# Kernel tuning notes

Hardware: AMD Instinct MI355X
Metric: run time of the kernel (lower is better)

## Reference

```python
import jax, jax.numpy as jnp
import numpy as np

B, S, D, H = 2, 2048, 1024, 16
DK = D // H  # 64


def setup_inputs() -> dict:
    key = jax.random.key(0)
    ks = jax.random.split(key, 12)
    def lin(kw, kb, fan_in, shape_w):
        bound = 1.0 / np.sqrt(fan_in)
        W = jax.random.uniform(kw, shape_w, jnp.float32, -bound, bound)
        b = jax.random.uniform(kb, (shape_w[0],), jnp.float32, -bound, bound)
        return W, b
    Q = jax.random.normal(ks[0], (B, S, D), jnp.float32)
    K = jax.random.normal(ks[1], (B, S, D), jnp.float32)
    V = jax.random.normal(ks[2], (B, S, D), jnp.float32)
    attn_mask = jax.random.randint(ks[3], (B, S, S), 0, 2) == 1  # bool, True=masked
    Wq, bq = lin(ks[4], ks[5], D, (D, D))
    Wk, bk = lin(ks[6], ks[7], D, (D, D))
    Wv, bv = lin(ks[8], ks[9], D, (D, D))
    Wo, bo = lin(ks[10], ks[11], D, (D, D))
    return {"Q": Q, "K": K, "V": V, "attn_mask": attn_mask,
            "Wq": Wq, "bq": bq, "Wk": Wk, "bk": bk,
            "Wv": Wv, "bv": bv, "Wo": Wo, "bo": bo}


def reference(Q, K, V, attn_mask, Wq, bq, Wk, bk, Wv, bv, Wo, bo):
    b, s, d = Q.shape
    # project and split heads: [B,S,D] -> [B,H,S,DK]
    def heads(x, W, bias):
        y = x @ W.T + bias
        return y.reshape(b, -1, H, DK).transpose(0, 2, 1, 3)
    q = heads(Q, Wq, bq)
    k = heads(K, Wk, bk)
    v = heads(V, Wv, bv)
    # scaled dot-product attention with custom reweighting
    scores = jnp.einsum('bhqd,bhkd->bhqk', q, k) / np.sqrt(DK).astype(jnp.float32)
    scores = jnp.where(attn_mask[:, None, :, :], jnp.float32(-1e9), scores)
    attn_weights = jax.nn.softmax(scores, axis=-1) * scores.shape[-1]  # non-standard *S_k scale
    ctx = jnp.einsum('bhqk,bhkd->bhqd', attn_weights, v)
    ctx = ctx.transpose(0, 2, 1, 3).reshape(b, -1, H * DK)
    output = ctx @ Wo.T + bo
    return output, attn_weights
```

## Files before the change

kernel.cpp:

```cpp
#include <hip/hip_runtime.h>
#include <hip/hip_bf16.h>
#include <type_traits>

typedef __bf16 bf16_t;
typedef __attribute__((ext_vector_type(8))) __bf16 bf16x8;
typedef __attribute__((ext_vector_type(4))) float f32x4;

#define B_ 2
#define S_ 2048
#define D_ 1024
#define H_ 16
#define DK_ 64

enum { OM_F32 = 0, OM_BF16 = 1, OM_SPLIT = 2, OM_HEADT = 3 };

__device__ inline void split8(const float* __restrict__ p, bf16x8& h, bf16x8& l) {
    float4 x0 = *(const float4*)p;
    float4 x1 = *(const float4*)(p + 4);
    float xs[8] = {x0.x, x0.y, x0.z, x0.w, x1.x, x1.y, x1.z, x1.w};
#pragma unroll
    for (int i = 0; i < 8; ++i) {
        bf16_t hh = (bf16_t)xs[i];
        h[i] = hh;
        l[i] = (bf16_t)(xs[i] - (float)hh);
    }
}
__device__ inline void hi8(const float* __restrict__ p, bf16x8& h) {
    float4 x0 = *(const float4*)p;
    float4 x1 = *(const float4*)(p + 4);
    float xs[8] = {x0.x, x0.y, x0.z, x0.w, x1.x, x1.y, x1.z, x1.w};
#pragma unroll
    for (int i = 0; i < 8; ++i) h[i] = (bf16_t)xs[i];
}

template <typename AT, int OMODE, bool SPLIT>
__global__ __launch_bounds__(256) void gemm_bt(
    const AT* __restrict__ A,
    const float* __restrict__ W,
    const float* __restrict__ bias,
    void* __restrict__ Yp,
    void* __restrict__ Y2p,
    int M, int N, int K)
{
    const int NB = N >> 6;
    const int bm = blockIdx.x / NB;
    const int bn = blockIdx.x % NB;
    const int tid  = threadIdx.x;
    const int wave = tid >> 6;
    const int lane = tid & 63;
    const int l16  = lane & 15;
    const int quad = lane >> 4;
    const int wm = wave >> 1, wn = wave & 1;

    __shared__ bf16_t Ah[64][40];
    __shared__ bf16_t Wh[64][40];
    __shared__ bf16_t Al[SPLIT ? 64 : 1][40];
    __shared__ bf16_t Wl[SPLIT ? 64 : 1][40];

    const int srow = tid >> 2;
    const int scol = (tid & 3) * 8;

    f32x4 acc[2][2];
#pragma unroll
    for (int i = 0; i < 2; ++i)
#pragma unroll
        for (int j = 0; j < 2; ++j) acc[i][j] = (f32x4){0.f, 0.f, 0.f, 0.f};

    const AT*    Arow = A + (size_t)(bm * 64 + srow) * K + scol;
    const float* Wrow = W + (size_t)(bn * 64 + srow) * K + scol;

    for (int k0 = 0; k0 < K; k0 += 32) {
        if constexpr (std::is_same_v<AT, float>) {
            bf16x8 ah, al;
            if constexpr (SPLIT) {
                split8(Arow + k0, ah, al);
                *(bf16x8*)(&Al[srow][scol]) = al;
            } else {
                hi8(Arow + k0, ah);
            }
            *(bf16x8*)(&Ah[srow][scol]) = ah;
        } else {
            *(bf16x8*)(&Ah[srow][scol]) = *(const bf16x8*)(Arow + k0);
        }
        {
            bf16x8 wh, wl;
            if constexpr (SPLIT) {
                split8(Wrow + k0, wh, wl);
                *(bf16x8*)(&Wl[srow][scol]) = wl;
            } else {
                hi8(Wrow + k0, wh);
            }
            *(bf16x8*)(&Wh[srow][scol]) = wh;
        }
        __syncthreads();

        bf16x8 afh[2], bfh[2], afl[2], bfl[2];
#pragma unroll
        for (int mi = 0; mi < 2; ++mi) {
            afh[mi] = *(const bf16x8*)(&Ah[wm * 32 + mi * 16 + l16][quad * 8]);
            if constexpr (SPLIT)
                afl[mi] = *(const bf16x8*)(&Al[wm * 32 + mi * 16 + l16][quad * 8]);
        }
#pragma unroll
        for (int ni = 0; ni < 2; ++ni) {
            bfh[ni] = *(const bf16x8*)(&Wh[wn * 32 + ni * 16 + l16][quad * 8]);
            if constexpr (SPLIT)
                bfl[ni] = *(const bf16x8*)(&Wl[wn * 32 + ni * 16 + l16][quad * 8]);
        }

#pragma unroll
        for (int mi = 0; mi < 2; ++mi)
#pragma unroll
            for (int ni = 0; ni < 2; ++ni) {
                acc[mi][ni] = __builtin_amdgcn_mfma_f32_16x16x32_bf16(
                    afh[mi], bfh[ni], acc[mi][ni], 0, 0, 0);
                if constexpr (SPLIT) {
                    acc[mi][ni] = __builtin_amdgcn_mfma_f32_16x16x32_bf16(
                        afl[mi], bfh[ni], acc[mi][ni], 0, 0, 0);
                    acc[mi][ni] = __builtin_amdgcn_mfma_f32_16x16x32_bf16(
                        afh[mi], bfl[ni], acc[mi][ni], 0, 0, 0);
                }
            }
        __syncthreads();
    }

#pragma unroll
    for (int ni = 0; ni < 2; ++ni) {
        const int col = bn * 64 + wn * 32 + ni * 16 + l16;
        const float bv = bias[col];
#pragma unroll
        for (int mi = 0; mi < 2; ++mi) {
#pragma unroll
            for (int r = 0; r < 4; ++r) {
                const int row = bm * 64 + wm * 32 + mi * 16 + quad * 4 + r;
                const float v = acc[mi][ni][r] + bv;
                if constexpr (OMODE == OM_F32) {
                    ((float*)Yp)[(size_t)row * N + col] = v;
                } else if constexpr (OMODE == OM_BF16) {
                    ((bf16_t*)Yp)[(size_t)row * N + col] = (bf16_t)v;
                } else if constexpr (OMODE == OM_SPLIT) {
                    const bf16_t hh = (bf16_t)v;
                    ((bf16_t*)Yp)[(size_t)row * N + col] = hh;
                    ((bf16_t*)Y2p)[(size_t)row * N + col] = (bf16_t)(v - (float)hh);
                } else {
                    const int bb  = row >> 11;
                    const int ss  = row & (S_ - 1);
                    const int hh2 = col >> 6;
                    const int dk  = col & (DK_ - 1);
                    ((bf16_t*)Yp)[((size_t)((bb * H_ + hh2) * DK_ + dk) << 11) + ss] =
                        (bf16_t)v;
                }
            }
        }
    }
}

__global__ __launch_bounds__(256) void pack_mask(
    const int* __restrict__ mask,
    unsigned long long* __restrict__ pk)
{
    const size_t nwords = (size_t)B_ * S_ * S_ / 64;
    const int lane = threadIdx.x & 63;
    size_t w = (size_t)blockIdx.x * 4 + (threadIdx.x >> 6);
    const size_t stride = (size_t)gridDim.x * 4;
    for (; w < nwords; w += stride) {
        const int m = mask[w * 64 + lane];
        const unsigned long long bb = __ballot(m != 0);
        if (lane == 0) pk[w] = bb;
    }
}

__global__ __launch_bounds__(256) void attn_kernel(
    const bf16_t* __restrict__ qh_g,
    const bf16_t* __restrict__ ql_g,
    const bf16_t* __restrict__ kh_g,
    const bf16_t* __restrict__ kl_g,
    const bf16_t* __restrict__ vt_g,
    const unsigned* __restrict__ pm,
    float* __restrict__ wout,
    float* __restrict__ normbuf,
    bf16_t* __restrict__ ctx)
{
    const int bid = blockIdx.x;
    const int qt = bid & 31;
    const int h  = (bid >> 5) & 15;
    const int b  = bid >> 9;
    const int tid  = threadIdx.x;
    const int wave = tid >> 6;
    const int lane = tid & 63;
    const int l16  = lane & 15;
    const int quad = lane >> 4;

    const int q0 = qt * 64 + wave * 16;

    __shared__ bf16_t Kh[32][72];
    __shared__ bf16_t Kl[32][72];
    __shared__ bf16_t vT[64][40];
    __shared__ bf16_t wl[4][16][40];

    const size_t qoff = ((size_t)(b * S_ + q0 + l16)) * D_ + h * DK_ + quad * 8;
    const bf16x8 qh0 = *(const bf16x8*)(qh_g + qoff);
    const bf16x8 qh1 = *(const bf16x8*)(qh_g + qoff + 32);
    const bf16x8 ql0 = *(const bf16x8*)(ql_g + qoff);
    const bf16x8 ql1 = *(const bf16x8*)(ql_g + qoff + 32);

    const float scale = 0.125f;

    const int srow  = tid >> 3;
    const int scol  = (tid & 7) * 8;
    const int srow2 = tid >> 2;
    const int scol2 = (tid & 3) * 8;
    const bf16_t* khst = kh_g + (size_t)b * S_ * D_ + h * DK_;
    const bf16_t* klst = kl_g + (size_t)b * S_ * D_ + h * DK_;
    const bf16_t* vtst = vt_g + ((size_t)(b * H_ + h) * DK_ + srow2) * S_ + scol2;

    const unsigned* pmrow = pm + (size_t)b * S_ * (S_ / 32);
    const size_t wbase = ((size_t)(b * H_ + h)) * S_ * S_;

    float lsum[4] = {0.f, 0.f, 0.f, 0.f};
    f32x4 acc[4];
#pragma unroll
    for (int t = 0; t < 4; ++t) acc[t] = (f32x4){0.f, 0.f, 0.f, 0.f};

    for (int j0 = 0; j0 < S_; j0 += 32) {
        {
            const size_t ko = (size_t)(j0 + srow) * D_ + scol;
            *(bf16x8*)(&Kh[srow][scol]) = *(const bf16x8*)(khst + ko);
            *(bf16x8*)(&Kl[srow][scol]) = *(const bf16x8*)(klst + ko);
            *(bf16x8*)(&vT[srow2][scol2]) = *(const bf16x8*)(vtst + j0);
        }
        unsigned mw[4];
#pragma unroll
        for (int r = 0; r < 4; ++r) {
            const int q = q0 + quad * 4 + r;
            mw[r] = pmrow[(size_t)q * (S_ / 32) + (j0 >> 5)];
        }
        __syncthreads();

#pragma unroll
        for (int sub = 0; sub < 2; ++sub) {
            const int rr = sub * 16 + l16;
            const bf16x8 kh0 = *(const bf16x8*)(&Kh[rr][quad * 8]);
            const bf16x8 kh1 = *(const bf16x8*)(&Kh[rr][32 + quad * 8]);
            const bf16x8 kl0 = *(const bf16x8*)(&Kl[rr][quad * 8]);
            const bf16x8 kl1 = *(const bf16x8*)(&Kl[rr][32 + quad * 8]);
            f32x4 c = (f32x4){0.f, 0.f, 0.f, 0.f};
            c = __builtin_amdgcn_mfma_f32_16x16x32_bf16(qh0, kh0, c, 0, 0, 0);
            c = __builtin_amdgcn_mfma_f32_16x16x32_bf16(qh1, kh1, c, 0, 0, 0);
            c = __builtin_amdgcn_mfma_f32_16x16x32_bf16(ql0, kh0, c, 0, 0, 0);
            c = __builtin_amdgcn_mfma_f32_16x16x32_bf16(ql1, kh1, c, 0, 0, 0);
            c = __builtin_amdgcn_mfma_f32_16x16x32_bf16(qh0, kl0, c, 0, 0, 0);
            c = __builtin_amdgcn_mfma_f32_16x16x32_bf16(qh1, kl1, c, 0, 0, 0);
            const int jt = j0 + sub * 16;
#pragma unroll
            for (int r = 0; r < 4; ++r) {
                const int q = q0 + quad * 4 + r;
                const int msk = (mw[r] >> (sub * 16 + l16)) & 1;
                const float e = msk ? 0.f : __expf(c[r] * scale);
                lsum[r] += e;
                __builtin_nontemporal_store(e, &wout[wbase + (size_t)q * S_ + jt + l16]);
                wl[wave][quad * 4 + r][sub * 16 + l16] = (bf16_t)e;
            }
        }
        const bf16x8 wa = *(const bf16x8*)(&wl[wave][l16][quad * 8]);
#pragma unroll
        for (int t = 0; t < 4; ++t) {
            const bf16x8 vf = *(const bf16x8*)(&vT[t * 16 + l16][quad * 8]);
            acc[t] = __builtin_amdgcn_mfma_f32_16x16x32_bf16(wa, vf, acc[t], 0, 0, 0);
        }
        __syncthreads();
    }

#pragma unroll
    for (int r = 0; r < 4; ++r) {
        float v = lsum[r];
        v += __shfl_xor(v, 1);
        v += __shfl_xor(v, 2);
        v += __shfl_xor(v, 4);
        v += __shfl_xor(v, 8);
        lsum[r] = v;
    }
    float norm[4];
#pragma unroll
    for (int r = 0; r < 4; ++r) norm[r] = 2048.f / lsum[r];

    if (l16 == 0) {
#pragma unroll
        for (int r = 0; r < 4; ++r)
            normbuf[(size_t)(b * H_ + h) * S_ + q0 + quad * 4 + r] = norm[r];
    }

#pragma unroll
    for (int t = 0; t < 4; ++t) {
#pragma unroll
        for (int r = 0; r < 4; ++r) {
            const int q = q0 + quad * 4 + r;
            ctx[((size_t)(b * S_ + q)) * D_ + h * DK_ + t * 16 + l16] =
                (bf16_t)(acc[t][r] * norm[r]);
        }
    }
}

__global__ __launch_bounds__(256) void rescale_wout(
    float* __restrict__ wout,
    const float* __restrict__ normbuf)
{
    const size_t total = (size_t)B_ * H_ * S_ * (S_ / 4);
    f32x4* wp = (f32x4*)wout;
    for (size_t i = (size_t)blockIdx.x * blockDim.x + threadIdx.x;
         i < total;
         i += (size_t)gridDim.x * blockDim.x) {
        const float n = normbuf[i >> 9];
        f32x4 w = __builtin_nontemporal_load(wp + i);
        w *= n;
        __builtin_nontemporal_store(w, wp + i);
    }
}

extern "C" void kernel_launch(void* const* d_in, const int* in_sizes, int n_in,
                              void* d_out, int out_size, void* d_ws, size_t ws_size,
                              hipStream_t stream) {
    const float* Q    = (const float*)d_in[0];
    const float* K    = (const float*)d_in[1];
    const float* V    = (const float*)d_in[2];
    const int*   mask = (const int*)d_in[3];
    const float* Wq   = (const float*)d_in[4];
    const float* bq   = (const float*)d_in[5];
    const float* Wk   = (const float*)d_in[6];
    const float* bk   = (const float*)d_in[7];
    const float* Wv   = (const float*)d_in[8];
    const float* bv   = (const float*)d_in[9];
    const float* Wo   = (const float*)d_in[10];
    const float* bo   = (const float*)d_in[11];

    const size_t BSD = (size_t)B_ * S_ * D_;
    float* out  = (float*)d_out;
    float* wout = out + BSD;

    bf16_t* qh = (bf16_t*)d_ws;
    bf16_t* ql = qh + BSD;
    bf16_t* kh = ql + BSD;
    bf16_t* kl = kh + BSD;
    bf16_t* vt = kl + BSD;
    bf16_t* cx = vt + BSD;
    unsigned long long* pk = (unsigned long long*)(cx + BSD);
    float* normbuf = (float*)((unsigned*)pk + (size_t)B_ * S_ * (S_ / 32));

    const int M = B_ * S_;
    const int N = D_;
    const int Kd = D_;
    const dim3 ggrid((M / 64) * (N / 64));
    const dim3 gblk(256);

    pack_mask<<<dim3(512), gblk, 0, stream>>>(mask, pk);

    gemm_bt<float, OM_SPLIT, true><<<ggrid, gblk, 0, stream>>>(Q, Wq, bq, qh, ql, M, N, Kd);
    gemm_bt<float, OM_SPLIT, true><<<ggrid, gblk, 0, stream>>>(K, Wk, bk, kh, kl, M, N, Kd);
    gemm_bt<float, OM_HEADT, false><<<ggrid, gblk, 0, stream>>>(V, Wv, bv, vt, nullptr, M, N, Kd);

    attn_kernel<<<dim3(B_ * H_ * (S_ / 64)), gblk, 0, stream>>>(
        qh, ql, kh, kl, vt, (const unsigned*)pk, wout, normbuf, cx);

    gemm_bt<bf16_t, OM_F32, false><<<ggrid, gblk, 0, stream>>>(cx, Wo, bo, out, nullptr, M, N, Kd);

    rescale_wout<<<dim3(2048), gblk, 0, stream>>>(wout, normbuf);
}
```

Before: 1.065 ms.

## Split attention into score and PV kernels, fuse weight rescale into PV pass

```diff
diff --git a/kernel.cpp b/kernel.cpp
--- a/kernel.cpp
+++ b/kernel.cpp
@@ -56,6 +56,7 @@
     __shared__ bf16_t Wh[64][40];
     __shared__ bf16_t Al[SPLIT ? 64 : 1][40];
     __shared__ bf16_t Wl[SPLIT ? 64 : 1][40];
+    __shared__ bf16_t T[OMODE == OM_HEADT ? 64 : 1][72];
 
     const int srow = tid >> 2;
     const int scol = (tid & 3) * 8;
@@ -122,6 +123,33 @@
                 }
             }
         __syncthreads();
+    }
+
+    if constexpr (OMODE == OM_HEADT) {
+#pragma unroll
+        for (int ni = 0; ni < 2; ++ni) {
+            const int cl = wn * 32 + ni * 16 + l16;
+            const float bv = bias[bn * 64 + cl];
+#pragma unroll
+            for (int mi = 0; mi < 2; ++mi)
+#pragma unroll
+                for (int r = 0; r < 4; ++r) {
+                    const int rl = wm * 32 + mi * 16 + quad * 4 + r;
+                    T[cl][rl] = (bf16_t)(acc[mi][ni][r] + bv);
+                }
+        }
+        __syncthreads();
+        const int bb  = bm >> 5;
+        const int ss0 = (bm * 64) & (S_ - 1);
+#pragma unroll
+        for (int it = 0; it < 2; ++it) {
+            const int dk = it * 32 + (tid >> 3);
+            const int so = (tid & 7) * 8;
+            *(bf16x8*)((bf16_t*)Yp +
+                ((size_t)((bb * H_ + bn) * DK_ + dk) << 11) + ss0 + so) =
+                *(const bf16x8*)(&T[dk][so]);
+        }
+        return;
     }
 
 #pragma unroll
@@ -142,13 +170,6 @@
                     const bf16_t hh = (bf16_t)v;
                     ((bf16_t*)Yp)[(size_t)row * N + col] = hh;
                     ((bf16_t*)Y2p)[(size_t)row * N + col] = (bf16_t)(v - (float)hh);
-                } else {
-                    const int bb  = row >> 11;
-                    const int ss  = row & (S_ - 1);
-                    const int hh2 = col >> 6;
-                    const int dk  = col & (DK_ - 1);
-                    ((bf16_t*)Yp)[((size_t)((bb * H_ + hh2) * DK_ + dk) << 11) + ss] =
-                        (bf16_t)v;
                 }
             }
         }
@@ -170,16 +191,14 @@
     }
 }
 
-__global__ __launch_bounds__(256) void attn_kernel(
+__global__ __launch_bounds__(256) void attn_scores(
     const bf16_t* __restrict__ qh_g,
     const bf16_t* __restrict__ ql_g,
     const bf16_t* __restrict__ kh_g,
     const bf16_t* __restrict__ kl_g,
-    const bf16_t* __restrict__ vt_g,
-    const unsigned* __restrict__ pm,
+    const unsigned long long* __restrict__ pm,
     float* __restrict__ wout,
-    float* __restrict__ normbuf,
-    bf16_t* __restrict__ ctx)
+    float* __restrict__ normbuf)
 {
     const int bid = blockIdx.x;
     const int qt = bid & 31;
@@ -193,10 +212,8 @@
 
     const int q0 = qt * 64 + wave * 16;
 
-    __shared__ bf16_t Kh[32][72];
-    __shared__ bf16_t Kl[32][72];
-    __shared__ bf16_t vT[64][40];
-    __shared__ bf16_t wl[4][16][40];
+    __shared__ bf16_t Kh[64][72];
+    __shared__ bf16_t Kl[64][72];
 
     const size_t qoff = ((size_t)(b * S_ + q0 + l16)) * D_ + h * DK_ + quad * 8;
     const bf16x8 qh0 = *(const bf16x8*)(qh_g + qoff);
@@ -206,39 +223,34 @@
 
     const float scale = 0.125f;
 
-    const int srow  = tid >> 3;
-    const int scol  = (tid & 7) * 8;
-    const int srow2 = tid >> 2;
-    const int scol2 = (tid & 3) * 8;
+    const int srow = tid >> 2;
+    const int scol = (tid & 3) * 16;
     const bf16_t* khst = kh_g + (size_t)b * S_ * D_ + h * DK_;
     const bf16_t* klst = kl_g + (size_t)b * S_ * D_ + h * DK_;
-    const bf16_t* vtst = vt_g + ((size_t)(b * H_ + h) * DK_ + srow2) * S_ + scol2;
-
-    const unsigned* pmrow = pm + (size_t)b * S_ * (S_ / 32);
+
+    const unsigned long long* pmrow = pm + (size_t)b * S_ * (S_ / 64);
     const size_t wbase = ((size_t)(b * H_ + h)) * S_ * S_;
 
     float lsum[4] = {0.f, 0.f, 0.f, 0.f};
-    f32x4 acc[4];
-#pragma unroll
-    for (int t = 0; t < 4; ++t) acc[t] = (f32x4){0.f, 0.f, 0.f, 0.f};
-
-    for (int j0 = 0; j0 < S_; j0 += 32) {
+
+    for (int j0 = 0; j0 < S_; j0 += 64) {
         {
             const size_t ko = (size_t)(j0 + srow) * D_ + scol;
-            *(bf16x8*)(&Kh[srow][scol]) = *(const bf16x8*)(khst + ko);
-            *(bf16x8*)(&Kl[srow][scol]) = *(const bf16x8*)(klst + ko);
-            *(bf16x8*)(&vT[srow2][scol2]) = *(const bf16x8*)(vtst + j0);
-        }
-        unsigned mw[4];
+            *(bf16x8*)(&Kh[srow][scol])     = *(const bf16x8*)(khst + ko);
+            *(bf16x8*)(&Kh[srow][scol + 8]) = *(const bf16x8*)(khst + ko + 8);
+            *(bf16x8*)(&Kl[srow][scol])     = *(const bf16x8*)(klst + ko);
+            *(bf16x8*)(&Kl[srow][scol + 8]) = *(const bf16x8*)(klst + ko + 8);
+        }
+        unsigned long long mw[4];
 #pragma unroll
         for (int r = 0; r < 4; ++r) {
             const int q = q0 + quad * 4 + r;
-            mw[r] = pmrow[(size_t)q * (S_ / 32) + (j0 >> 5)];
-        }
-        __syncthreads();
-
-#pragma unroll
-        for (int sub = 0; sub < 2; ++sub) {
+            mw[r] = pmrow[(size_t)q * (S_ / 64) + (j0 >> 6)];
+        }
+        __syncthreads();
+
+#pragma unroll
+        for (int sub = 0; sub < 4; ++sub) {
             const int rr = sub * 16 + l16;
             const bf16x8 kh0 = *(const bf16x8*)(&Kh[rr][quad * 8]);
             const bf16x8 kh1 = *(const bf16x8*)(&Kh[rr][32 + quad * 8]);
@@ -255,18 +267,11 @@
 #pragma unroll
             for (int r = 0; r < 4; ++r) {
                 const int q = q0 + quad * 4 + r;
-                const int msk = (mw[r] >> (sub * 16 + l16)) & 1;
+                const int msk = (int)((mw[r] >> (sub * 16 + l16)) & 1ull);
                 const float e = msk ? 0.f : __expf(c[r] * scale);
                 lsum[r] += e;
                 __builtin_nontemporal_store(e, &wout[wbase + (size_t)q * S_ + jt + l16]);
-                wl[wave][quad * 4 + r][sub * 16 + l16] = (bf16_t)e;
-            }
-        }
-        const bf16x8 wa = *(const bf16x8*)(&wl[wave][l16][quad * 8]);
-#pragma unroll
-        for (int t = 0; t < 4; ++t) {
-            const bf16x8 vf = *(const bf16x8*)(&vT[t * 16 + l16][quad * 8]);
-            acc[t] = __builtin_amdgcn_mfma_f32_16x16x32_bf16(wa, vf, acc[t], 0, 0, 0);
+            }
         }
         __syncthreads();
     }
@@ -280,14 +285,84 @@
         v += __shfl_xor(v, 8);
         lsum[r] = v;
     }
-    float norm[4];
-#pragma unroll
-    for (int r = 0; r < 4; ++r) norm[r] = 2048.f / lsum[r];
-
     if (l16 == 0) {
 #pragma unroll
         for (int r = 0; r < 4; ++r)
-            normbuf[(size_t)(b * H_ + h) * S_ + q0 + quad * 4 + r] = norm[r];
+            normbuf[(size_t)(b * H_ + h) * S_ + q0 + quad * 4 + r] = 2048.f / lsum[r];
+    }
+}
+
+__global__ __launch_bounds__(256) void attn_pv(
+    const bf16_t* __restrict__ vt_g,
+    const float*  __restrict__ normbuf,
+    float* __restrict__ wout,
+    bf16_t* __restrict__ ctx)
+{
+    const int bid = blockIdx.x;
+    const int qt = bid & 31;
+    const int h  = (bid >> 5) & 15;
+    const int b  = bid >> 9;
+    const int tid  = threadIdx.x;
+    const int wave = tid >> 6;
+    const int lane = tid & 63;
+    const int l16  = lane & 15;
+    const int quad = lane >> 4;
+
+    const int q0 = qt * 64 + wave * 16;
+
+    __shared__ bf16_t vT[64][72];
+
+    const int sdk = tid >> 2;
+    const int sjo = (tid & 3) * 16;
+    const bf16_t* vtst = vt_g + ((size_t)(b * H_ + h) * DK_ + sdk) * S_ + sjo;
+
+    const size_t wbase = ((size_t)(b * H_ + h)) * S_ * S_;
+    const float nrmA = normbuf[(size_t)(b * H_ + h) * S_ + q0 + l16];
+    float norm_c[4];
+#pragma unroll
+    for (int r = 0; r < 4; ++r)
+        norm_c[r] = normbuf[(size_t)(b * H_ + h) * S_ + q0 + quad * 4 + r];
+
+    f32x4 acc[4];
+#pragma unroll
+    for (int t = 0; t < 4; ++t) acc[t] = (f32x4){0.f, 0.f, 0.f, 0.f};
+
+    float* wrow = wout + wbase + (size_t)(q0 + l16) * S_;
+
+    for (int j0 = 0; j0 < S_; j0 += 64) {
+        {
+            *(bf16x8*)(&vT[sdk][sjo])     = *(const bf16x8*)(vtst + j0);
+            *(bf16x8*)(&vT[sdk][sjo + 8]) = *(const bf16x8*)(vtst + j0 + 8);
+        }
+        __syncthreads();
+
+#pragma unroll
+        for (int half = 0; half < 2; ++half) {
+            const int jj = j0 + half * 32 + quad * 8;
+            float* ep = wrow + jj;
+            float4 e0, e1;
+            e0.x = __builtin_nontemporal_load(ep + 0);
+            e0.y = __builtin_nontemporal_load(ep + 1);
+            e0.z = __builtin_nontemporal_load(ep + 2);
+            e0.w = __builtin_nontemporal_load(ep + 3);
+            e1.x = __builtin_nontemporal_load(ep + 4);
+            e1.y = __builtin_nontemporal_load(ep + 5);
+            e1.z = __builtin_nontemporal_load(ep + 6);
+            e1.w = __builtin_nontemporal_load(ep + 7);
+            const float es[8] = {e0.x, e0.y, e0.z, e0.w, e1.x, e1.y, e1.z, e1.w};
+            bf16x8 wa;
+#pragma unroll
+            for (int i = 0; i < 8; ++i) {
+                __builtin_nontemporal_store(es[i] * nrmA, ep + i);
+                wa[i] = (bf16_t)es[i];
+            }
+#pragma unroll
+            for (int t = 0; t < 4; ++t) {
+                const bf16x8 vf = *(const bf16x8*)(&vT[t * 16 + l16][half * 32 + quad * 8]);
+                acc[t] = __builtin_amdgcn_mfma_f32_16x16x32_bf16(wa, vf, acc[t], 0, 0, 0);
+            }
+        }
+        __syncthreads();
     }
 
 #pragma unroll
@@ -296,24 +371,8 @@
         for (int r = 0; r < 4; ++r) {
             const int q = q0 + quad * 4 + r;
             ctx[((size_t)(b * S_ + q)) * D_ + h * DK_ + t * 16 + l16] =
-                (bf16_t)(acc[t][r] * norm[r]);
-        }
-    }
-}
-
-__global__ __launch_bounds__(256) void rescale_wout(
-    float* __restrict__ wout,
-    const float* __restrict__ normbuf)
-{
-    const size_t total = (size_t)B_ * H_ * S_ * (S_ / 4);
-    f32x4* wp = (f32x4*)wout;
-    for (size_t i = (size_t)blockIdx.x * blockDim.x + threadIdx.x;
-         i < total;
-         i += (size_t)gridDim.x * blockDim.x) {
-        const float n = normbuf[i >> 9];
-        f32x4 w = __builtin_nontemporal_load(wp + i);
-        w *= n;
-        __builtin_nontemporal_store(w, wp + i);
+                (bf16_t)(acc[t][r] * norm_c[r]);
+        }
     }
 }
 
@@ -344,7 +403,7 @@
     bf16_t* vt = kl + BSD;
     bf16_t* cx = vt + BSD;
     unsigned long long* pk = (unsigned long long*)(cx + BSD);
-    float* normbuf = (float*)((unsigned*)pk + (size_t)B_ * S_ * (S_ / 32));
+    float* normbuf = (float*)(pk + (size_t)B_ * S_ * (S_ / 64));
 
     const int M = B_ * S_;
     const int N = D_;
@@ -358,10 +417,11 @@
     gemm_bt<float, OM_SPLIT, true><<<ggrid, gblk, 0, stream>>>(K, Wk, bk, kh, kl, M, N, Kd);
     gemm_bt<float, OM_HEADT, false><<<ggrid, gblk, 0, stream>>>(V, Wv, bv, vt, nullptr, M, N, Kd);
 
-    attn_kernel<<<dim3(B_ * H_ * (S_ / 64)), gblk, 0, stream>>>(
-        qh, ql, kh, kl, vt, (const unsigned*)pk, wout, normbuf, cx);
+    attn_scores<<<dim3(B_ * H_ * (S_ / 64)), gblk, 0, stream>>>(
+        qh, ql, kh, kl, pk, wout, normbuf);
+
+    attn_pv<<<dim3(B_ * H_ * (S_ / 64)), gblk, 0, stream>>>(
+        vt, normbuf, wout, cx);
 
     gemm_bt<bf16_t, OM_F32, false><<<ggrid, gblk, 0, stream>>>(cx, Wo, bo, out, nullptr, M, N, Kd);
-
-    rescale_wout<<<dim3(2048), gblk, 0, stream>>>(wout, normbuf);
-}
+}
```

Result: slower. 1.130 ms (+6.1%).
